# Optimization experiments

Hardware: AMD Instinct MI355X
Metric: run time of the kernel (lower is better)

The kernel has to match this reference:

```python
import jax, jax.numpy as jnp
from jax import lax
import numpy as np

L = 8  # db4 filter length
DEC_LO = np.array([-0.010597401784997278, 0.032883011666982945, 0.030841381835986965,
                   -0.18703481171888114, -0.02798376941698385, 0.6308807679295904,
                   0.7148465705525415, 0.23037781330885523], dtype=np.float32)
DEC_HI = np.array([-0.23037781330885523, 0.7148465705525415, -0.6308807679295904,
                   -0.02798376941698385, 0.18703481171888114, 0.030841381835986965,
                   -0.032883011666982945, -0.010597401784997278], dtype=np.float32)
# analysis: correlation kernels are time-reversed decomposition filters (as in pytorch_wavelets)
AF = np.stack([DEC_LO[::-1], DEC_HI[::-1]])  # (2, L)
# synthesis: torch conv_transpose(rec_filt) == lhs-dilated correlation with flip(rec) = dec
SF = np.stack([DEC_LO, DEC_HI])              # (2, L)


def _afb1d(x, axis):
    # analysis filter bank along `axis` of (B, C, H, W); symmetric pad, stride 2
    B, C = x.shape[0], x.shape[1]
    N = x.shape[axis]
    outsize = (N + L - 1) // 2           # pywt symmetric coeff length
    p = 2 * (outsize - 1) - N + L        # total pad
    pad = [(0, 0)] * 4
    pad[axis] = (p // 2, (p + 1) // 2)
    xp = jnp.pad(x, pad, mode='symmetric')
    if axis == 2:
        kern, strides = AF.reshape(2, 1, L, 1), (2, 1)
    else:
        kern, strides = AF.reshape(2, 1, 1, L), (1, 2)
    kern = jnp.asarray(np.tile(kern, (C, 1, 1, 1)), dtype=x.dtype)  # (2C,1,kh,kw)
    return lax.conv_general_dilated(xp, kern, strides, 'VALID',
                                    dimension_numbers=('NCHW', 'OIHW', 'NCHW'),
                                    feature_group_count=C)


def dwt2d(x):
    # single-level 2D db4 DWT, symmetric mode (pytorch_wavelets DWTForward J=1)
    B, C = x.shape[0], x.shape[1]
    lohi = _afb1d(x, 3)                  # (B, 2C, H, W'); ch = c*2 + band_w
    y = _afb1d(lohi, 2)                  # (B, 4C, H', W'); ch = c*4 + band_w*2 + band_h
    y = y.reshape(B, C, 4, y.shape[-2], y.shape[-1])
    return y[:, :, 0], y[:, :, 1:]       # ll (B,C,H',W'), highs (B,C,3,H',W')


def _sfb1d(lo, hi, axis):
    # synthesis filter bank along `axis`: upsample-by-2 transposed conv, crop L-2
    C = lo.shape[1]
    if axis == 2:
        k0, k1 = SF[0].reshape(1, 1, L, 1), SF[1].reshape(1, 1, L, 1)
        dil, pad = (2, 1), [(1, 1), (0, 0)]   # lax pad = (L-1) - (L-2) = 1
    else:
        k0, k1 = SF[0].reshape(1, 1, 1, L), SF[1].reshape(1, 1, 1, L)
        dil, pad = (1, 2), [(0, 0), (1, 1)]
    k0 = jnp.asarray(np.tile(k0, (C, 1, 1, 1)), dtype=lo.dtype)
    k1 = jnp.asarray(np.tile(k1, (C, 1, 1, 1)), dtype=lo.dtype)
    conv = lambda v, k: lax.conv_general_dilated(
        v, k, (1, 1), pad, lhs_dilation=dil,
        dimension_numbers=('NCHW', 'OIHW', 'NCHW'), feature_group_count=C)
    return conv(lo, k0) + conv(hi, k1)


def idwt2d(ll, lh, hl, hh):
    lo = _sfb1d(ll, lh, 2)
    hi = _sfb1d(hl, hh, 2)
    return _sfb1d(lo, hi, 3)


def setup_inputs() -> dict:
    key = jax.random.key(0)
    ks = jax.random.split(key, 5)
    B, Cin, Cout, H, W = 16, 64, 64, 128, 128
    m = (H + L - 1) // 2                 # 67 wavelet modes per axis
    scale = 1.0 / (Cin * Cout)
    x = jax.random.normal(ks[0], (B, Cin, H, W), dtype=jnp.float32)
    ws = {f"w{i + 1}": scale * jax.random.uniform(ks[i + 1], (Cin, Cout, m, m), dtype=jnp.float32)
          for i in range(4)}
    return {"x": x, **ws}


def reference(x, w1, w2, w3, w4):
    ll, highs = dwt2d(x)
    mix = lambda v, w: jnp.einsum('bixy,ioxy->boxy', v, w)  # per-mode channel mixing
    out_ll = mix(ll, w1)
    lh = mix(highs[:, :, 0], w2)
    hl = mix(highs[:, :, 1], w3)
    hh = mix(highs[:, :, 2], w4)
    return idwt2d(out_ll, lh, hl, hh)
```

## Files before the change

### kernel.cpp

```cpp
#include <hip/hip_runtime.h>

#define BB 16
#define CC 64
#define HH 128
#define WW 128
#define MM 67
#define MODES (MM*MM)
#define MC 32
#define NCHUNK 141

typedef float f4 __attribute__((ext_vector_type(4)));

__constant__ float DEC_LO[8] = {-0.010597401784997278f, 0.032883011666982945f, 0.030841381835986965f,
                                -0.18703481171888114f, -0.02798376941698385f, 0.6308807679295904f,
                                0.7148465705525415f, 0.23037781330885523f};
__constant__ float DEC_HI[8] = {-0.23037781330885523f, 0.7148465705525415f, -0.6308807679295904f,
                                -0.02798376941698385f, 0.18703481171888114f, 0.030841381835986965f,
                                -0.032883011666982945f, -0.010597401784997278f};

__global__ __launch_bounds__(256, 2) void dwt_f(const float* __restrict__ x, float* __restrict__ cf) {
    __shared__ float st[2][HH][MM];
    const int bc  = blockIdx.x;
    const int tid = threadIdx.x;
    const float* xr = x + (size_t)bc * HH * WW;

    for (int p = tid; p < HH * MM; p += 256) {
        int wo = p % MM, h = p / MM;
        const float* row = xr + h * WW;
        float lo = 0.f, hi = 0.f;
        int base = 2 * wo - 6;
        #pragma unroll
        for (int k = 0; k < 8; ++k) {
            int i = base + k;
            i = (i < 0) ? (-i - 1) : i;
            i = (i >= WW) ? (2 * WW - 1 - i) : i;
            float v = row[i];
            lo += v * DEC_LO[7 - k];
            hi += v * DEC_HI[7 - k];
        }
        st[0][h][wo] = lo;
        st[1][h][wo] = hi;
    }
    __syncthreads();

    const int NH2 = (MM + 1) / 2;
    float* cfo = cf + (size_t)bc * 4 * MODES;
    for (int q = tid; q < NH2 * MM; q += 256) {
        int wo = q % MM, hp = q / MM;
        int ho0 = 2 * hp, ho1 = 2 * hp + 1;
        #pragma unroll
        for (int fw = 0; fw < 2; ++fw) {
            float rv[10];
            #pragma unroll
            for (int k = 0; k < 10; ++k) {
                int i = 4 * hp - 6 + k;
                i = (i < 0) ? (-i - 1) : i;
                i = (i >= HH) ? (2 * HH - 1 - i) : i;
                rv[k] = st[fw][i][wo];
            }
            float lo0 = 0.f, hi0 = 0.f, lo1 = 0.f, hi1 = 0.f;
            #pragma unroll
            for (int k = 0; k < 8; ++k) {
                lo0 += rv[k]     * DEC_LO[7 - k];
                hi0 += rv[k]     * DEC_HI[7 - k];
                lo1 += rv[k + 2] * DEC_LO[7 - k];
                hi1 += rv[k + 2] * DEC_HI[7 - k];
            }
            float* b0 = cfo + (size_t)(fw * 2 + 0) * MODES;
            float* b1 = cfo + (size_t)(fw * 2 + 1) * MODES;
            b0[ho0 * MM + wo] = lo0;
            b1[ho0 * MM + wo] = hi0;
            if (ho1 < MM) {
                b0[ho1 * MM + wo] = lo1;
                b1[ho1 * MM + wo] = hi1;
            }
        }
    }
}

__global__ __launch_bounds__(256, 2) void mix_k(const float* __restrict__ cf,
                                                const float* __restrict__ w1,
                                                const float* __restrict__ w2,
                                                const float* __restrict__ w3,
                                                const float* __restrict__ w4,
                                                float* __restrict__ out) {
    __shared__ float sc[8][CC][MC];
    const int d   = blockIdx.x;
    const int cyc = d >> 4, r = d & 15;
    const int g   = cyc * 8 + (r & 7);
    const int bh  = r >> 3;
    if (g >= 4 * NCHUNK) return;
    const int band = g / NCHUNK;
    const int m0   = min((g % NCHUNK) * MC, MODES - MC);
    const int tid  = threadIdx.x;
    const int bg0  = bh * 8;
    const float* w = (band == 0) ? w1 : (band == 1) ? w2 : (band == 2) ? w3 : w4;

    {
        const int c = tid & 7, r0 = tid >> 3;
        #pragma unroll
        for (int p = 0; p < 16; ++p) {
            int rr = r0 + (p << 5);
            int b = bg0 + (rr >> 6), i = rr & 63;
            f4 v = *(const f4*)(cf + ((size_t)((b * CC + i) * 4) + band) * MODES + m0 + c * 4);
            *(f4*)&sc[rr >> 6][i][c * 4] = v;
        }
    }
    __syncthreads();

    const int lane = tid & 63, wv = tid >> 6;
    const int o2 = wv * 8 + (lane >> 3);
    const int mc4 = (lane & 7) * 4;
    const size_t IST = (size_t)CC * MODES;
    const float* wpl = w + (size_t)o2 * MODES + m0 + mc4;
    const float* wph = wpl + (size_t)32 * MODES;

    f4 accL[8], accH[8];
    #pragma unroll
    for (int b = 0; b < 8; ++b) { accL[b] = (f4)(0.f); accH[b] = (f4)(0.f); }

    f4 al0, al1, al2, al3, ah0, ah1, ah2, ah3;
    f4 bl0, bl1, bl2, bl3, bh0, bh1, bh2, bh3;
    al0 = *(const f4*)(wpl + 0 * IST);  ah0 = *(const f4*)(wph + 0 * IST);
    al1 = *(const f4*)(wpl + 1 * IST);  ah1 = *(const f4*)(wph + 1 * IST);
    al2 = *(const f4*)(wpl + 2 * IST);  ah2 = *(const f4*)(wph + 2 * IST);
    al3 = *(const f4*)(wpl + 3 * IST);  ah3 = *(const f4*)(wph + 3 * IST);

    #pragma unroll 1
    for (int ib = 0; ib < 64; ib += 8) {
        bl0 = *(const f4*)(wpl + (size_t)(ib + 4) * IST);  bh0 = *(const f4*)(wph + (size_t)(ib + 4) * IST);
        bl1 = *(const f4*)(wpl + (size_t)(ib + 5) * IST);  bh1 = *(const f4*)(wph + (size_t)(ib + 5) * IST);
        bl2 = *(const f4*)(wpl + (size_t)(ib + 6) * IST);  bh2 = *(const f4*)(wph + (size_t)(ib + 6) * IST);
        bl3 = *(const f4*)(wpl + (size_t)(ib + 7) * IST);  bh3 = *(const f4*)(wph + (size_t)(ib + 7) * IST);
        #pragma unroll
        for (int b = 0; b < 8; ++b) {
            f4 s = *(const f4*)&sc[b][ib + 0][mc4];
            accL[b] += s * al0;  accH[b] += s * ah0;
        }
        #pragma unroll
        for (int b = 0; b < 8; ++b) {
            f4 s = *(const f4*)&sc[b][ib + 1][mc4];
            accL[b] += s * al1;  accH[b] += s * ah1;
        }
        #pragma unroll
        for (int b = 0; b < 8; ++b) {
            f4 s = *(const f4*)&sc[b][ib + 2][mc4];
            accL[b] += s * al2;  accH[b] += s * ah2;
        }
        #pragma unroll
        for (int b = 0; b < 8; ++b) {
            f4 s = *(const f4*)&sc[b][ib + 3][mc4];
            accL[b] += s * al3;  accH[b] += s * ah3;
        }
        if (ib + 8 < 64) {
            al0 = *(const f4*)(wpl + (size_t)(ib + 8)  * IST);  ah0 = *(const f4*)(wph + (size_t)(ib + 8)  * IST);
            al1 = *(const f4*)(wpl + (size_t)(ib + 9)  * IST);  ah1 = *(const f4*)(wph + (size_t)(ib + 9)  * IST);
            al2 = *(const f4*)(wpl + (size_t)(ib + 10) * IST);  ah2 = *(const f4*)(wph + (size_t)(ib + 10) * IST);
            al3 = *(const f4*)(wpl + (size_t)(ib + 11) * IST);  ah3 = *(const f4*)(wph + (size_t)(ib + 11) * IST);
        }
        #pragma unroll
        for (int b = 0; b < 8; ++b) {
            f4 s = *(const f4*)&sc[b][ib + 4][mc4];
            accL[b] += s * bl0;  accH[b] += s * bh0;
        }
        #pragma unroll
        for (int b = 0; b < 8; ++b) {
            f4 s = *(const f4*)&sc[b][ib + 5][mc4];
            accL[b] += s * bl1;  accH[b] += s * bh1;
        }
        #pragma unroll
        for (int b = 0; b < 8; ++b) {
            f4 s = *(const f4*)&sc[b][ib + 6][mc4];
            accL[b] += s * bl2;  accH[b] += s * bh2;
        }
        #pragma unroll
        for (int b = 0; b < 8; ++b) {
            f4 s = *(const f4*)&sc[b][ib + 7][mc4];
            accL[b] += s * bl3;  accH[b] += s * bh3;
        }
    }

    #pragma unroll
    for (int b = 0; b < 8; ++b) {
        *(f4*)&out[((size_t)(((bg0 + b) * CC + o2) * 4) + band) * MODES + m0 + mc4] = accL[b];
        *(f4*)&out[((size_t)(((bg0 + b) * CC + o2 + 32) * 4) + band) * MODES + m0 + mc4] = accH[b];
    }
}

__global__ __launch_bounds__(256, 2) void idwt_f(const float* __restrict__ mx, float* __restrict__ out) {
    __shared__ float su[2][HH][MM];
    const int bc  = blockIdx.x;
    const int tid = threadIdx.x;
    const float* mxb = mx + (size_t)bc * 4 * MODES;

    for (int p = tid; p < 2 * (HH / 2) * MM; p += 256) {
        int wo = p % MM;
        int a  = (p / MM) % (HH / 2);
        int fw = p / (MM * (HH / 2));
        const float* lo = mxb + (size_t)(fw * 2) * MODES + wo;
        const float* hi = lo + MODES;
        float l[4], h4[4];
        #pragma unroll
        for (int q = 0; q < 4; ++q) {
            l[q]  = lo[(a + q) * MM];
            h4[q] = hi[(a + q) * MM];
        }
        float o0 = 0.f, o1 = 0.f;
        #pragma unroll
        for (int q = 0; q < 4; ++q) {
            o0 += l[q] * DEC_LO[2 * q + 1] + h4[q] * DEC_HI[2 * q + 1];
            o1 += l[q] * DEC_LO[2 * q]     + h4[q] * DEC_HI[2 * q];
        }
        su[fw][2 * a][wo]     = o0;
        su[fw][2 * a + 1][wo] = o1;
    }
    __syncthreads();

    float* ob = out + (size_t)bc * HH * WW;
    for (int p = tid; p < HH * (WW / 2); p += 256) {
        int a = p & 63, h = p >> 6;
        float l[4], h4[4];
        #pragma unroll
        for (int q = 0; q < 4; ++q) {
            l[q]  = su[0][h][a + q];
            h4[q] = su[1][h][a + q];
        }
        float o0 = 0.f, o1 = 0.f;
        #pragma unroll
        for (int q = 0; q < 4; ++q) {
            o0 += l[q] * DEC_LO[2 * q + 1] + h4[q] * DEC_HI[2 * q + 1];
            o1 += l[q] * DEC_LO[2 * q]     + h4[q] * DEC_HI[2 * q];
        }
        *(float2*)&ob[h * WW + 2 * a] = make_float2(o0, o1);
    }
}

extern "C" void kernel_launch(void* const* d_in, const int* in_sizes, int n_in,
                              void* d_out, int out_size, void* d_ws, size_t ws_size,
                              hipStream_t stream) {
    const float* x  = (const float*)d_in[0];
    const float* w1 = (const float*)d_in[1];
    const float* w2 = (const float*)d_in[2];
    const float* w3 = (const float*)d_in[3];
    const float* w4 = (const float*)d_in[4];
    float* out = (float*)d_out;

    const size_t COEFF_FLTS = (size_t)BB * CC * 4 * MODES;
    float* buf1 = (float*)d_ws;
    float* buf2 = buf1 + COEFF_FLTS;

    dwt_f<<<BB * CC, 256, 0, stream>>>(x, buf1);
    mix_k<<<1136, 256, 0, stream>>>(buf1, w1, w2, w3, w4, buf2);
    idwt_f<<<BB * CC, 256, 0, stream>>>(buf2, out);
}
```

Measured before the change: 262.0 us.

## Restructure mix kernel: all batches per block, split-K over input channels, XCD remap

The mixing kernel now gives each 512-thread block all 16 batches for a 16-mode chunk, so each weight element is read once instead of twice (previously two batch halves each loaded the same weights). The input-channel reduction is split across two halves of the block and combined through shared memory. Block indices are remapped so that consecutive chunks land on the same XCD for L2 locality. The explicit software prefetch of weights is dropped in favour of a simple unrolled loop, and the extra reduction pass and barrier add some overhead.

```diff
diff --git a/kernel.cpp b/kernel.cpp
--- a/kernel.cpp
+++ b/kernel.cpp
@@ -6,8 +6,8 @@
 #define WW 128
 #define MM 67
 #define MODES (MM*MM)
-#define MC 32
-#define NCHUNK 141
+#define MC2 16
+#define NCH2 281
 
 typedef float f4 __attribute__((ext_vector_type(4)));
 
@@ -78,112 +78,85 @@
     }
 }
 
-__global__ __launch_bounds__(256, 2) void mix_k(const float* __restrict__ cf,
+__global__ __launch_bounds__(512, 4) void mix_k(const float* __restrict__ cf,
                                                 const float* __restrict__ w1,
                                                 const float* __restrict__ w2,
                                                 const float* __restrict__ w3,
                                                 const float* __restrict__ w4,
                                                 float* __restrict__ out) {
-    __shared__ float sc[8][CC][MC];
-    const int d   = blockIdx.x;
-    const int cyc = d >> 4, r = d & 15;
-    const int g   = cyc * 8 + (r & 7);
-    const int bh  = r >> 3;
-    if (g >= 4 * NCHUNK) return;
-    const int band = g / NCHUNK;
-    const int m0   = min((g % NCHUNK) * MC, MODES - MC);
+    __shared__ float sc[BB][CC][MC2];
+    int flat = blockIdx.y * NCH2 + blockIdx.x;
+    {
+        const int q = 1124 / 8, r = 1124 % 8;
+        int xcd = flat & 7, j = flat >> 3;
+        flat = (xcd < r ? xcd * (q + 1) : r * (q + 1) + (xcd - r) * q) + j;
+    }
+    const int band = flat / NCH2;
+    const int m0   = min((flat % NCH2) * MC2, MODES - MC2);
     const int tid  = threadIdx.x;
-    const int bg0  = bh * 8;
     const float* w = (band == 0) ? w1 : (band == 1) ? w2 : (band == 2) ? w3 : w4;
 
     {
-        const int c = tid & 7, r0 = tid >> 3;
-        #pragma unroll
-        for (int p = 0; p < 16; ++p) {
-            int rr = r0 + (p << 5);
-            int b = bg0 + (rr >> 6), i = rr & 63;
-            f4 v = *(const f4*)(cf + ((size_t)((b * CC + i) * 4) + band) * MODES + m0 + c * 4);
-            *(f4*)&sc[rr >> 6][i][c * 4] = v;
+        const int c = tid & 3, r0 = tid >> 2;
+        #pragma unroll
+        for (int p = 0; p < 8; ++p) {
+            int r = r0 + (p << 7);
+            f4 v = *(const f4*)(cf + ((size_t)(r * 4) + band) * MODES + m0 + c * 4);
+            *(f4*)&sc[r >> 6][r & 63][c * 4] = v;
         }
     }
     __syncthreads();
 
     const int lane = tid & 63, wv = tid >> 6;
-    const int o2 = wv * 8 + (lane >> 3);
-    const int mc4 = (lane & 7) * 4;
+    const int m4 = lane & 3;
+    const int bh = lane >> 5;
+    const int op = (wv & 3) * 8 + ((lane >> 2) & 7);
+    const int ih = wv >> 2;
+    const int b0 = bh * 8;
     const size_t IST = (size_t)CC * MODES;
-    const float* wpl = w + (size_t)o2 * MODES + m0 + mc4;
+    const float* wpl = w + ((size_t)(ih * 32) * CC + op) * MODES + m0 + m4 * 4;
     const float* wph = wpl + (size_t)32 * MODES;
 
     f4 accL[8], accH[8];
     #pragma unroll
     for (int b = 0; b < 8; ++b) { accL[b] = (f4)(0.f); accH[b] = (f4)(0.f); }
 
-    f4 al0, al1, al2, al3, ah0, ah1, ah2, ah3;
-    f4 bl0, bl1, bl2, bl3, bh0, bh1, bh2, bh3;
-    al0 = *(const f4*)(wpl + 0 * IST);  ah0 = *(const f4*)(wph + 0 * IST);
-    al1 = *(const f4*)(wpl + 1 * IST);  ah1 = *(const f4*)(wph + 1 * IST);
-    al2 = *(const f4*)(wpl + 2 * IST);  ah2 = *(const f4*)(wph + 2 * IST);
-    al3 = *(const f4*)(wpl + 3 * IST);  ah3 = *(const f4*)(wph + 3 * IST);
-
-    #pragma unroll 1
-    for (int ib = 0; ib < 64; ib += 8) {
-        bl0 = *(const f4*)(wpl + (size_t)(ib + 4) * IST);  bh0 = *(const f4*)(wph + (size_t)(ib + 4) * IST);
-        bl1 = *(const f4*)(wpl + (size_t)(ib + 5) * IST);  bh1 = *(const f4*)(wph + (size_t)(ib + 5) * IST);
-        bl2 = *(const f4*)(wpl + (size_t)(ib + 6) * IST);  bh2 = *(const f4*)(wph + (size_t)(ib + 6) * IST);
-        bl3 = *(const f4*)(wpl + (size_t)(ib + 7) * IST);  bh3 = *(const f4*)(wph + (size_t)(ib + 7) * IST);
-        #pragma unroll
-        for (int b = 0; b < 8; ++b) {
-            f4 s = *(const f4*)&sc[b][ib + 0][mc4];
-            accL[b] += s * al0;  accH[b] += s * ah0;
-        }
-        #pragma unroll
-        for (int b = 0; b < 8; ++b) {
-            f4 s = *(const f4*)&sc[b][ib + 1][mc4];
-            accL[b] += s * al1;  accH[b] += s * ah1;
-        }
-        #pragma unroll
-        for (int b = 0; b < 8; ++b) {
-            f4 s = *(const f4*)&sc[b][ib + 2][mc4];
-            accL[b] += s * al2;  accH[b] += s * ah2;
-        }
-        #pragma unroll
-        for (int b = 0; b < 8; ++b) {
-            f4 s = *(const f4*)&sc[b][ib + 3][mc4];
-            accL[b] += s * al3;  accH[b] += s * ah3;
-        }
-        if (ib + 8 < 64) {
-            al0 = *(const f4*)(wpl + (size_t)(ib + 8)  * IST);  ah0 = *(const f4*)(wph + (size_t)(ib + 8)  * IST);
-            al1 = *(const f4*)(wpl + (size_t)(ib + 9)  * IST);  ah1 = *(const f4*)(wph + (size_t)(ib + 9)  * IST);
-            al2 = *(const f4*)(wpl + (size_t)(ib + 10) * IST);  ah2 = *(const f4*)(wph + (size_t)(ib + 10) * IST);
-            al3 = *(const f4*)(wpl + (size_t)(ib + 11) * IST);  ah3 = *(const f4*)(wph + (size_t)(ib + 11) * IST);
-        }
-        #pragma unroll
-        for (int b = 0; b < 8; ++b) {
-            f4 s = *(const f4*)&sc[b][ib + 4][mc4];
-            accL[b] += s * bl0;  accH[b] += s * bh0;
-        }
-        #pragma unroll
-        for (int b = 0; b < 8; ++b) {
-            f4 s = *(const f4*)&sc[b][ib + 5][mc4];
-            accL[b] += s * bl1;  accH[b] += s * bh1;
-        }
-        #pragma unroll
-        for (int b = 0; b < 8; ++b) {
-            f4 s = *(const f4*)&sc[b][ib + 6][mc4];
-            accL[b] += s * bl2;  accH[b] += s * bh2;
-        }
-        #pragma unroll
-        for (int b = 0; b < 8; ++b) {
-            f4 s = *(const f4*)&sc[b][ib + 7][mc4];
-            accL[b] += s * bl3;  accH[b] += s * bh3;
-        }
-    }
-
-    #pragma unroll
-    for (int b = 0; b < 8; ++b) {
-        *(f4*)&out[((size_t)(((bg0 + b) * CC + o2) * 4) + band) * MODES + m0 + mc4] = accL[b];
-        *(f4*)&out[((size_t)(((bg0 + b) * CC + o2 + 32) * 4) + band) * MODES + m0 + mc4] = accH[b];
+    const int ibase = ih * 32;
+    #pragma unroll 2
+    for (int ii = 0; ii < 32; ++ii) {
+        f4 wl = *(const f4*)wpl;  wpl += IST;
+        f4 wh = *(const f4*)wph;  wph += IST;
+        const int i = ibase + ii;
+        #pragma unroll
+        for (int b = 0; b < 8; ++b) {
+            f4 s = *(const f4*)&sc[b0 + b][i][m4 * 4];
+            accL[b] += s * wl;
+            accH[b] += s * wh;
+        }
+    }
+
+    __syncthreads();
+    float* scratch = &sc[0][0][0];
+    const int key = tid & 255;
+    if (ih == 1) {
+        #pragma unroll
+        for (int b = 0; b < 8; ++b) {
+            *(f4*)&scratch[(size_t)(b * 256 + key) * 4]       = accL[b];
+            *(f4*)&scratch[(size_t)((8 + b) * 256 + key) * 4] = accH[b];
+        }
+    }
+    __syncthreads();
+    if (ih == 0) {
+        #pragma unroll
+        for (int b = 0; b < 8; ++b) {
+            accL[b] += *(const f4*)&scratch[(size_t)(b * 256 + key) * 4];
+            accH[b] += *(const f4*)&scratch[(size_t)((8 + b) * 256 + key) * 4];
+        }
+        #pragma unroll
+        for (int b = 0; b < 8; ++b) {
+            *(f4*)&out[((size_t)(((b0 + b) * CC + op) * 4) + band) * MODES + m0 + m4 * 4]      = accL[b];
+            *(f4*)&out[((size_t)(((b0 + b) * CC + op + 32) * 4) + band) * MODES + m0 + m4 * 4] = accH[b];
+        }
     }
 }
 
@@ -250,6 +223,9 @@
     float* buf2 = buf1 + COEFF_FLTS;
 
     dwt_f<<<BB * CC, 256, 0, stream>>>(x, buf1);
-    mix_k<<<1136, 256, 0, stream>>>(buf1, w1, w2, w3, w4, buf2);
+    {
+        dim3 grid(NCH2, 4);
+        mix_k<<<grid, 512, 0, stream>>>(buf1, w1, w2, w3, w4, buf2);
+    }
     idwt_f<<<BB * CC, 256, 0, stream>>>(buf2, out);
 }
```

New measurement: 248.7 us. 1.05x faster.
